# Optimization experiments

Hardware: AMD Instinct MI355X
Metric: run time of the kernel (lower is better)

## Reference

```python
import jax, jax.numpy as jnp
import numpy as np

N = 65536
PT_DIM = 3
ENC_DIM = 512
P = 4096
RADIUS = 0.05
ALPHA = 6.0
SQRT_D = ENC_DIM ** 0.5


def setup_inputs() -> dict:
    key = jax.random.key(0)
    k1, k2, k3 = jax.random.split(key, 3)
    pts = jax.random.normal(k1, (N, PT_DIM), dtype=jnp.float32)
    # Frozen random-feature projection matrices (strict_standard_normal ~ randn)
    A = jax.random.normal(k2, (PT_DIM, ENC_DIM), dtype=jnp.float32) * ALPHA
    B = jax.random.normal(k3, (PT_DIM, P), dtype=jnp.float32) * 1.8
    return {"pts": pts, "A": A, "B": B}


def reference(pts, A, B):
    x = pts / RADIUS                      # (N, 3)
    pA = x @ A                            # (N, d)
    pB = x @ B                            # (N, p)
    cA, sA = jnp.cos(pA), jnp.sin(pA)     # (N, d) each
    eA = jnp.concatenate([cA, sA], axis=-1)          # (N, 2d)
    eB = jnp.concatenate([jnp.cos(pB), jnp.sin(pB)], axis=-1)  # (N, 2p)
    # G = eB @ (eB^T @ eA): contract over N first (small 2p x 2d matrix)
    M = eB.T @ eA                         # (2p, 2d)
    G = eB @ M                            # (N, 2d)
    Gc, Gs = G[:, :ENC_DIM], G[:, ENC_DIM:]
    # complex divide (Gc + i Gs) / (cA + i sA); |cA + i sA|^2 == 1
    den = cA * cA + sA * sA
    re = (Gc * cA + Gs * sA) / den
    im = (Gs * cA - Gc * sA) / den
    # L2-normalize the complex vector per point, scale by sqrt(d)
    nrm = jnp.sqrt(jnp.sum(re * re + im * im, axis=-1, keepdims=True))
    scale = SQRT_D / nrm
    # return real/imag concatenated: (N, 2d)
    return jnp.concatenate([re * scale, im * scale], axis=-1)
```

## Files before the change

kernel.cpp:

```cpp
#include <hip/hip_runtime.h>
#include <hip/hip_bf16.h>
#include <math.h>

typedef __attribute__((ext_vector_type(8))) short bf16x8;
typedef __attribute__((ext_vector_type(4))) float f32x4;

constexpr int NPTS = 65536;
constexpr int ENC  = 512;
constexpr int P    = 4096;
constexpr int JD   = 1024;
constexpr int ID   = 8192;
constexpr int CH   = 8192;
constexpr int NCH  = NPTS / CH;
constexpr int LDK  = 8192;

constexpr float INV_R   = 20.0f;
constexpr float INV2PI  = 0.15915494309189535f;
constexpr float SQRT_D  = 22.627416997969522f;

__device__ __forceinline__ unsigned short f2bf(float f) {
    unsigned int u = __float_as_uint(f);
    u = (u + 0x7FFFu + ((u >> 16) & 1u)) >> 16;
    return (unsigned short)u;
}

__device__ __forceinline__ void sincos_rev(float p, float* s, float* c) {
    float r = p * INV2PI;
    r = r - floorf(r);
    *s = __builtin_amdgcn_sinf(r);
    *c = __builtin_amdgcn_cosf(r);
}

__device__ __forceinline__ void gload16(const void* g, void* l) {
    __builtin_amdgcn_global_load_lds(
        (const __attribute__((address_space(1))) unsigned int*)g,
        (__attribute__((address_space(3))) unsigned int*)l, 16, 0, 0);
}

__global__ __launch_bounds__(256)
void gen_t(const float* __restrict__ pts, const float* __restrict__ A,
           const float* __restrict__ B, unsigned short* __restrict__ eAT,
           unsigned short* __restrict__ eBT, int n0) {
    int idx = blockIdx.x * 256 + threadIdx.x;
    int nh  = idx & (CH / 2 - 1);
    int r   = idx >> 12;
    int nl  = nh * 2;
    int n   = n0 + nl;
    float x0a = pts[n * 3 + 0], x1a = pts[n * 3 + 1], x2a = pts[n * 3 + 2];
    float x0b = pts[n * 3 + 3], x1b = pts[n * 3 + 4], x2b = pts[n * 3 + 5];
    float w0, w1, w2;
    unsigned short *dc, *dsn;
    if (r < ENC) {
        w0 = A[r]; w1 = A[ENC + r]; w2 = A[2 * ENC + r];
        dc  = eAT + (size_t)r * CH + nl;
        dsn = eAT + (size_t)(r + ENC) * CH + nl;
    } else {
        int i = r - ENC;
        w0 = B[i]; w1 = B[P + i]; w2 = B[2 * P + i];
        dc  = eBT + (size_t)i * CH + nl;
        dsn = eBT + (size_t)(i + P) * CH + nl;
    }
    float pa = (x0a * w0 + x1a * w1 + x2a * w2) * INV_R;
    float pb = (x0b * w0 + x1b * w1 + x2b * w2) * INV_R;
    float sa, ca, sb, cb;
    sincos_rev(pa, &sa, &ca);
    sincos_rev(pb, &sb, &cb);
    ushort2 vc; vc.x = f2bf(ca); vc.y = f2bf(cb);
    ushort2 vs; vs.x = f2bf(sa); vs.y = f2bf(sb);
    *(ushort2*)dc  = vc;
    *(ushort2*)dsn = vs;
}

__global__ __launch_bounds__(256)
void gen_b(const float* __restrict__ pts, const float* __restrict__ B,
           unsigned short* __restrict__ eB, int n0) {
    int idx = blockIdx.x * 256 + threadIdx.x;
    int ih = idx & 2047;
    int ln = idx >> 11;
    int i  = ih * 2;
    int n  = n0 + ln;
    float x0 = pts[n * 3 + 0], x1 = pts[n * 3 + 1], x2 = pts[n * 3 + 2];
    float p0 = (x0 * B[i]     + x1 * B[P + i]     + x2 * B[2 * P + i])     * INV_R;
    float p1 = (x0 * B[i + 1] + x1 * B[P + i + 1] + x2 * B[2 * P + i + 1]) * INV_R;
    float s0, c0, s1, c1;
    sincos_rev(p0, &s0, &c0);
    sincos_rev(p1, &s1, &c1);
    ushort2 vc; vc.x = f2bf(c0); vc.y = f2bf(c1);
    ushort2 vs; vs.x = f2bf(s0); vs.y = f2bf(s1);
    *(ushort2*)(eB + (size_t)ln * ID + i)     = vc;
    *(ushort2*)(eB + (size_t)ln * ID + P + i) = vs;
}

template <int BM, int BN, int K, bool ACCUM>
__global__ __launch_bounds__(512, 2)
void gemm_nt(const unsigned short* __restrict__ Ag,
             const unsigned short* __restrict__ Bg,
             float* __restrict__ C, int ldc, int beta) {
    constexpr int BSZ = (BM + BN) * 64;
    constexpr int NA  = BM / 64;
    constexpr int NB  = BN / 64;
    constexpr int NT  = K / 64;
    static_assert(NA + NB == 6, "6 issues/K-tile assumed by vmcnt(6)");
    __shared__ __align__(16) unsigned short lds[3 * BSZ];

    const int tid  = threadIdx.x;
    const int wave = tid >> 6, lane = tid & 63;
    const int mr = lane & 15, q = lane >> 4;
    const int srow = tid >> 3, sslot = tid & 7;
    const int wm = (BM >= BN) ? (wave >> 1) * 64 : (wave & 1) * 64;
    const int wn = (BM >= BN) ? (wave & 1) * 64 : (wave >> 1) * 64;

    const int gx   = gridDim.x;
    const int nwg  = gx * gridDim.y;
    const int flat = blockIdx.y * gx + blockIdx.x;
    const int swz  = (flat & 7) * (nwg >> 3) + (flat >> 3);
    const int m0   = (swz % gx) * BM;
    const int n0   = (swz / gx) * BN;

    const char* aG = (const char*)Ag;
    const char* bG = (const char*)Bg;
    const int ssw = (sslot ^ (srow & 7)) * 16;
    size_t aoff[NA], boff[NB];
#pragma unroll
    for (int j = 0; j < NA; ++j)
        aoff[j] = (size_t)(m0 + j * 64 + srow) * (LDK * 2) + ssw;
#pragma unroll
    for (int j = 0; j < NB; ++j)
        boff[j] = (size_t)(n0 + j * 64 + srow) * (LDK * 2) + ssw;

    unsigned short* bufC  = lds;
    unsigned short* bufN  = lds + BSZ;
    unsigned short* bufN2 = lds + 2 * BSZ;

    auto stage = [&](int idx, unsigned short* buf, size_t kB) {
        if (idx < NA)
            gload16(aG + aoff[idx] + kB, buf + idx * 4096 + wave * 512);
        else
            gload16(bG + boff[idx - NA] + kB,
                    buf + BM * 64 + (idx - NA) * 4096 + wave * 512);
    };

    f32x4 acc[4][4];
#pragma unroll
    for (int a = 0; a < 4; ++a)
#pragma unroll
        for (int b = 0; b < 4; ++b) acc[a][b] = (f32x4){0.f, 0.f, 0.f, 0.f};

#pragma unroll
    for (int i = 0; i < 6; ++i) stage(i, bufC, 0);
#pragma unroll
    for (int i = 0; i < 6; ++i) stage(i, bufN, 128);
    asm volatile("s_waitcnt vmcnt(6)" ::: "memory");
    __builtin_amdgcn_s_barrier();
    __builtin_amdgcn_sched_barrier(0);

    size_t kPre = 256;
#pragma unroll 1
    for (int kt = 0; kt < NT; ++kt) {
        const bool pf = (kt + 2 < NT);
        bf16x8 af[2][4], bfr[2][4];
#pragma unroll
        for (int kk = 0; kk < 2; ++kk) {
#pragma unroll
            for (int mi = 0; mi < 4; ++mi) {
                int m = wm + mi * 16 + mr;
                af[kk][mi] = *(const bf16x8*)(bufC + m * 64 +
                                              (((kk * 4 + q) ^ (m & 7)) * 8));
            }
#pragma unroll
            for (int ni = 0; ni < 4; ++ni) {
                int n = wn + ni * 16 + mr;
                bfr[kk][ni] = *(const bf16x8*)(bufC + BM * 64 + n * 64 +
                                               (((kk * 4 + q) ^ (n & 7)) * 8));
            }
        }
        if (pf) {
#pragma unroll
            for (int i = 0; i < 6; ++i) stage(i, bufN2, kPre);
        }
        __builtin_amdgcn_s_setprio(1);
#pragma unroll
        for (int kk = 0; kk < 2; ++kk)
#pragma unroll
            for (int mi = 0; mi < 4; ++mi)
#pragma unroll
                for (int ni = 0; ni < 4; ++ni)
                    acc[mi][ni] = __builtin_amdgcn_mfma_f32_16x16x32_bf16(
                        af[kk][mi], bfr[kk][ni], acc[mi][ni], 0, 0, 0);
        __builtin_amdgcn_s_setprio(0);
        if (pf)                    asm volatile("s_waitcnt vmcnt(6)" ::: "memory");
        else if (kt + 1 < NT)      asm volatile("s_waitcnt vmcnt(0)" ::: "memory");
        __builtin_amdgcn_s_barrier();
        __builtin_amdgcn_sched_barrier(0);
        unsigned short* t = bufC; bufC = bufN; bufN = bufN2; bufN2 = t;
        kPre += 128;
    }

#pragma unroll
    for (int mi = 0; mi < 4; ++mi)
#pragma unroll
        for (int ni = 0; ni < 4; ++ni)
#pragma unroll
            for (int r = 0; r < 4; ++r) {
                int m = m0 + wm + mi * 16 + q * 4 + r;
                int n = n0 + wn + ni * 16 + mr;
                size_t off = (size_t)m * ldc + n;
                float v = acc[mi][ni][r];
                if (ACCUM) { if (beta) v += C[off]; }
                C[off] = v;
            }
}

__global__ __launch_bounds__(256)
void cvt(const float* __restrict__ src, unsigned short* __restrict__ dst) {
    int idx = blockIdx.x * 256 + threadIdx.x;
    float4 v = ((const float4*)src)[idx];
    ushort4 o;
    o.x = f2bf(v.x); o.y = f2bf(v.y); o.z = f2bf(v.z); o.w = f2bf(v.w);
    ((ushort4*)dst)[idx] = o;
}

__global__ __launch_bounds__(256)
void epi(float* __restrict__ out, const float* __restrict__ pts,
         const float* __restrict__ A) {
    int n = blockIdx.x;
    int t = threadIdx.x;
    float x0 = pts[n * 3 + 0], x1 = pts[n * 3 + 1], x2 = pts[n * 3 + 2];
    float* row = out + (size_t)n * JD;
    float reA[2], imA[2];
    float ssum = 0.f;
#pragma unroll
    for (int u = 0; u < 2; ++u) {
        int j = t + u * 256;
        float pa = (x0 * A[j] + x1 * A[ENC + j] + x2 * A[2 * ENC + j]) * INV_R;
        float s, c;
        sincos_rev(pa, &s, &c);
        float gc = row[j], gs = row[ENC + j];
        float re = gc * c + gs * s;
        float im = gs * c - gc * s;
        reA[u] = re; imA[u] = im;
        ssum += re * re + im * im;
    }
#pragma unroll
    for (int off = 32; off > 0; off >>= 1) ssum += __shfl_down(ssum, off);
    __shared__ float red[4];
    if ((t & 63) == 0) red[t >> 6] = ssum;
    __syncthreads();
    float tot = red[0] + red[1] + red[2] + red[3];
    float scale = SQRT_D / sqrtf(tot);
#pragma unroll
    for (int u = 0; u < 2; ++u) {
        int j = t + u * 256;
        row[j]       = reA[u] * scale;
        row[ENC + j] = imA[u] * scale;
    }
}

extern "C" void kernel_launch(void* const* d_in, const int* in_sizes, int n_in,
                              void* d_out, int out_size, void* d_ws, size_t ws_size,
                              hipStream_t stream) {
    const float* pts = (const float*)d_in[0];
    const float* A   = (const float*)d_in[1];
    const float* B   = (const float*)d_in[2];
    float* out = (float*)d_out;
    char* ws = (char*)d_ws;

    unsigned short* eAT = (unsigned short*)ws;
    unsigned short* eBT = (unsigned short*)(ws + (size_t)JD * CH * 2);
    unsigned short* eBw = (unsigned short*)ws;
    size_t offMT = (size_t)(JD + ID) * CH * 2;
    float* MTf = (float*)(ws + offMT);
    unsigned short* MTb = (unsigned short*)(ws + offMT + (size_t)JD * ID * 4);

    for (int c = 0; c < NCH; ++c) {
        gen_t<<<dim3(73728), 256, 0, stream>>>(pts, A, B, eAT, eBT, c * CH);
        gemm_nt<128, 256, CH, true><<<dim3(8, 32), 512, 0, stream>>>(
            eAT, eBT, MTf, ID, c);
    }
    cvt<<<dim3(8192), 256, 0, stream>>>(MTf, MTb);
    for (int c = 0; c < NCH; ++c) {
        gen_b<<<dim3(65536), 256, 0, stream>>>(pts, B, eBw, c * CH);
        gemm_nt<256, 128, ID, false><<<dim3(32, 8), 512, 0, stream>>>(
            eBw, MTb, out + (size_t)c * CH * JD, JD, 0);
    }
    epi<<<dim3(NPTS), 256, 0, stream>>>(out, pts, A);
}
```

Before: 3.278 ms.

## Use split-K GEMM with atomic accumulation for second-stage product

Replaces the second GEMM (8192x1024 output per chunk, K=8192) with a new kernel that splits K into two halves across blockIdx.z, uses 256x256 tiles with triple-buffered LDS and a grid swizzle, and accumulates partial results with float atomicAdd. Each chunk's output region is now zeroed by a separate kernel before the GEMM. The aim is more blocks in flight (256 instead of 256 smaller tiles with longer K) and better reuse from larger tiles. In exchange it adds atomic traffic and an extra memset pass over the output, and the atomics make the floating-point summation order nondeterministic.

```diff
diff --git a/kernel.cpp b/kernel.cpp
--- a/kernel.cpp
+++ b/kernel.cpp
@@ -211,6 +211,125 @@
             }
 }
 
+__global__ __launch_bounds__(512, 2)
+void gemm_sk(const unsigned short* __restrict__ Ag,
+             const unsigned short* __restrict__ Bg,
+             float* __restrict__ C, int ldc) {
+    constexpr int BK    = 32;
+    constexpr int BSZ   = 512 * BK;
+    constexpr int KHALF = 4096;
+    constexpr int NT    = KHALF / BK;
+    __shared__ __align__(16) unsigned short lds[3 * BSZ];
+
+    const int tid  = threadIdx.x;
+    const int wave = tid >> 6, lane = tid & 63;
+    const int mr = lane & 15, q = lane >> 4;
+    const int wm = (wave >> 1) * 64;
+    const int wn = (wave & 1) * 128;
+
+    const int flat = blockIdx.x + 32 * (blockIdx.y + 4 * blockIdx.z);
+    const int swz  = (flat & 7) * 32 + (flat >> 3);
+    const int m0   = (swz & 31) * 256;
+    const int rest = swz >> 5;
+    const int n0   = (rest & 3) * 256;
+    const int z    = rest >> 2;
+    const size_t kb0 = (size_t)z * KHALF * 2;
+
+    const int L  = tid >> 3;
+    const int S  = tid & 7;
+    const int u  = S ^ (L & 7);
+    const int grow = 2 * L + (u >> 2);
+    const int gk   = (u & 3) * 16;
+    const char* aG = (const char*)Ag;
+    const char* bG = (const char*)Bg;
+    size_t aoff[2], boff[2];
+#pragma unroll
+    for (int j = 0; j < 2; ++j) {
+        aoff[j] = (size_t)(m0 + j * 128 + grow) * (LDK * 2) + kb0 + gk;
+        boff[j] = (size_t)(n0 + j * 128 + grow) * (LDK * 2) + kb0 + gk;
+    }
+
+    unsigned short* bufC  = lds;
+    unsigned short* bufN  = lds + BSZ;
+    unsigned short* bufN2 = lds + 2 * BSZ;
+
+    auto stage = [&](int idx, unsigned short* buf, size_t kB) {
+        if (idx < 2)
+            gload16(aG + aoff[idx] + kB, buf + idx * 4096 + wave * 512);
+        else
+            gload16(bG + boff[idx - 2] + kB,
+                    buf + 8192 + (idx - 2) * 4096 + wave * 512);
+    };
+
+    f32x4 acc[4][8];
+#pragma unroll
+    for (int a = 0; a < 4; ++a)
+#pragma unroll
+        for (int b = 0; b < 8; ++b) acc[a][b] = (f32x4){0.f, 0.f, 0.f, 0.f};
+
+#pragma unroll
+    for (int i = 0; i < 4; ++i) stage(i, bufC, 0);
+#pragma unroll
+    for (int i = 0; i < 4; ++i) stage(i, bufN, 64);
+    asm volatile("s_waitcnt vmcnt(4)" ::: "memory");
+    __builtin_amdgcn_s_barrier();
+    __builtin_amdgcn_sched_barrier(0);
+
+    size_t kPre = 128;
+#pragma unroll 1
+    for (int kt = 0; kt < NT; ++kt) {
+        const bool pf = (kt + 2 < NT);
+        bf16x8 af[4], bfr[8];
+#pragma unroll
+        for (int mi = 0; mi < 4; ++mi) {
+            int m = wm + mi * 16 + mr, Lm = m >> 1;
+            af[mi] = *(const bf16x8*)(bufC + Lm * 64 +
+                                      ((((m & 1) * 4 + q) ^ (Lm & 7)) * 8));
+        }
+#pragma unroll
+        for (int ni = 0; ni < 8; ++ni) {
+            int n = wn + ni * 16 + mr, Ln = n >> 1;
+            bfr[ni] = *(const bf16x8*)(bufC + 8192 + Ln * 64 +
+                                       ((((n & 1) * 4 + q) ^ (Ln & 7)) * 8));
+        }
+        if (pf) {
+#pragma unroll
+            for (int i = 0; i < 4; ++i) stage(i, bufN2, kPre);
+        }
+        __builtin_amdgcn_s_setprio(1);
+#pragma unroll
+        for (int mi = 0; mi < 4; ++mi)
+#pragma unroll
+            for (int ni = 0; ni < 8; ++ni)
+                acc[mi][ni] = __builtin_amdgcn_mfma_f32_16x16x32_bf16(
+                    af[mi], bfr[ni], acc[mi][ni], 0, 0, 0);
+        __builtin_amdgcn_s_setprio(0);
+        if (pf)                    asm volatile("s_waitcnt vmcnt(4)" ::: "memory");
+        else if (kt + 1 < NT)      asm volatile("s_waitcnt vmcnt(0)" ::: "memory");
+        __builtin_amdgcn_s_barrier();
+        __builtin_amdgcn_sched_barrier(0);
+        unsigned short* t = bufC; bufC = bufN; bufN = bufN2; bufN2 = t;
+        kPre += 64;
+    }
+
+#pragma unroll
+    for (int mi = 0; mi < 4; ++mi)
+#pragma unroll
+        for (int ni = 0; ni < 8; ++ni)
+#pragma unroll
+            for (int r = 0; r < 4; ++r) {
+                int m = m0 + wm + mi * 16 + q * 4 + r;
+                int n = n0 + wn + ni * 16 + mr;
+                atomicAdd(&C[(size_t)m * ldc + n], acc[mi][ni][r]);
+            }
+}
+
+__global__ __launch_bounds__(256)
+void zerof(float4* __restrict__ p) {
+    int idx = blockIdx.x * 256 + threadIdx.x;
+    p[idx] = (float4){0.f, 0.f, 0.f, 0.f};
+}
+
 __global__ __launch_bounds__(256)
 void cvt(const float* __restrict__ src, unsigned short* __restrict__ dst) {
     int idx = blockIdx.x * 256 + threadIdx.x;
@@ -280,8 +399,10 @@
     cvt<<<dim3(8192), 256, 0, stream>>>(MTf, MTb);
     for (int c = 0; c < NCH; ++c) {
         gen_b<<<dim3(65536), 256, 0, stream>>>(pts, B, eBw, c * CH);
-        gemm_nt<256, 128, ID, false><<<dim3(32, 8), 512, 0, stream>>>(
-            eBw, MTb, out + (size_t)c * CH * JD, JD, 0);
+        zerof<<<dim3(8192), 256, 0, stream>>>(
+            (float4*)(out + (size_t)c * CH * JD));
+        gemm_sk<<<dim3(32, 4, 2), 512, 0, stream>>>(
+            eBw, MTb, out + (size_t)c * CH * JD, JD);
     }
     epi<<<dim3(NPTS), 256, 0, stream>>>(out, pts, A);
 }
```

After: 3.367 ms. 2.7% more time.

## Quantize first GEMM operands to int8 and use i8 MFMA

Applied to the files above, without the earlier changes.

The sin/cos features feeding the M = eB^T eA reduction over points are now quantized to int8 with scale 127 instead of bf16, and a new int8 MFMA GEMM (16x16x64) accumulates into int32. The int32 result is rescaled by 1/127^2 when it is converted to bf16 for the second GEMM. This halves operand bytes and uses the higher-throughput int8 matrix path for the first GEMM, at the cost of coarser precision (about 7 bits) in the features.

```diff
diff --git a/kernel.cpp b/kernel.cpp
--- a/kernel.cpp
+++ b/kernel.cpp
@@ -4,6 +4,7 @@
 
 typedef __attribute__((ext_vector_type(8))) short bf16x8;
 typedef __attribute__((ext_vector_type(4))) float f32x4;
+typedef __attribute__((ext_vector_type(4))) int   i32x4;
 
 constexpr int NPTS = 65536;
 constexpr int ENC  = 512;
@@ -17,6 +18,7 @@
 constexpr float INV_R   = 20.0f;
 constexpr float INV2PI  = 0.15915494309189535f;
 constexpr float SQRT_D  = 22.627416997969522f;
+constexpr float INV_Q2  = 1.0f / (127.0f * 127.0f);
 
 __device__ __forceinline__ unsigned short f2bf(float f) {
     unsigned int u = __float_as_uint(f);
@@ -39,8 +41,8 @@
 
 __global__ __launch_bounds__(256)
 void gen_t(const float* __restrict__ pts, const float* __restrict__ A,
-           const float* __restrict__ B, unsigned short* __restrict__ eAT,
-           unsigned short* __restrict__ eBT, int n0) {
+           const float* __restrict__ B, signed char* __restrict__ eAT,
+           signed char* __restrict__ eBT, int n0) {
     int idx = blockIdx.x * 256 + threadIdx.x;
     int nh  = idx & (CH / 2 - 1);
     int r   = idx >> 12;
@@ -49,7 +51,7 @@
     float x0a = pts[n * 3 + 0], x1a = pts[n * 3 + 1], x2a = pts[n * 3 + 2];
     float x0b = pts[n * 3 + 3], x1b = pts[n * 3 + 4], x2b = pts[n * 3 + 5];
     float w0, w1, w2;
-    unsigned short *dc, *dsn;
+    signed char *dc, *dsn;
     if (r < ENC) {
         w0 = A[r]; w1 = A[ENC + r]; w2 = A[2 * ENC + r];
         dc  = eAT + (size_t)r * CH + nl;
@@ -65,10 +67,13 @@
     float sa, ca, sb, cb;
     sincos_rev(pa, &sa, &ca);
     sincos_rev(pb, &sb, &cb);
-    ushort2 vc; vc.x = f2bf(ca); vc.y = f2bf(cb);
-    ushort2 vs; vs.x = f2bf(sa); vs.y = f2bf(sb);
-    *(ushort2*)dc  = vc;
-    *(ushort2*)dsn = vs;
+    char2 vc, vs;
+    vc.x = (signed char)__float2int_rn(ca * 127.0f);
+    vc.y = (signed char)__float2int_rn(cb * 127.0f);
+    vs.x = (signed char)__float2int_rn(sa * 127.0f);
+    vs.y = (signed char)__float2int_rn(sb * 127.0f);
+    *(char2*)dc  = vc;
+    *(char2*)dsn = vs;
 }
 
 __global__ __launch_bounds__(256)
@@ -91,6 +96,121 @@
     *(ushort2*)(eB + (size_t)ln * ID + P + i) = vs;
 }
 
+__global__ __launch_bounds__(512, 2)
+void gemm_i8(const signed char* __restrict__ Ag,
+             const signed char* __restrict__ Bg,
+             int* __restrict__ C, int ldc, int beta) {
+    constexpr int BSZB = (128 + 256) * 128;
+    constexpr int NT   = 8192 / 128;
+    __shared__ __align__(16) signed char lds[3 * BSZB];
+
+    const int tid  = threadIdx.x;
+    const int wave = tid >> 6, lane = tid & 63;
+    const int mr = lane & 15, q = lane >> 4;
+    const int srow = tid >> 3, sslot = tid & 7;
+    const int wm = (wave & 1) * 64, wn = (wave >> 1) * 64;
+
+    const int gx   = gridDim.x;
+    const int nwg  = gx * gridDim.y;
+    const int flat = blockIdx.y * gx + blockIdx.x;
+    const int swz  = (flat & 7) * (nwg >> 3) + (flat >> 3);
+    const int m0   = (swz % gx) * 128;
+    const int n0   = (swz / gx) * 256;
+
+    const char* aG = (const char*)Ag;
+    const char* bG = (const char*)Bg;
+    const int ssw = (sslot ^ (srow & 7)) * 16;
+    size_t aoff[2], boff[4];
+#pragma unroll
+    for (int j = 0; j < 2; ++j)
+        aoff[j] = (size_t)(m0 + j * 64 + srow) * LDK + ssw;
+#pragma unroll
+    for (int j = 0; j < 4; ++j)
+        boff[j] = (size_t)(n0 + j * 64 + srow) * LDK + ssw;
+
+    signed char* bufC  = lds;
+    signed char* bufN  = lds + BSZB;
+    signed char* bufN2 = lds + 2 * BSZB;
+
+    auto stage = [&](int idx, signed char* buf, size_t kB) {
+        if (idx < 2)
+            gload16(aG + aoff[idx] + kB, buf + idx * 8192 + tid * 16);
+        else
+            gload16(bG + boff[idx - 2] + kB,
+                    buf + 16384 + (idx - 2) * 8192 + tid * 16);
+    };
+
+    i32x4 acc[4][4];
+#pragma unroll
+    for (int a = 0; a < 4; ++a)
+#pragma unroll
+        for (int b = 0; b < 4; ++b) acc[a][b] = (i32x4){0, 0, 0, 0};
+
+#pragma unroll
+    for (int i = 0; i < 6; ++i) stage(i, bufC, 0);
+#pragma unroll
+    for (int i = 0; i < 6; ++i) stage(i, bufN, 128);
+    asm volatile("s_waitcnt vmcnt(6)" ::: "memory");
+    __builtin_amdgcn_s_barrier();
+    __builtin_amdgcn_sched_barrier(0);
+
+    size_t kPre = 256;
+#pragma unroll 1
+    for (int kt = 0; kt < NT; ++kt) {
+        const bool pf = (kt + 2 < NT);
+        i32x4 af[2][4], bfr[2][4];
+#pragma unroll
+        for (int kk = 0; kk < 2; ++kk) {
+#pragma unroll
+            for (int mi = 0; mi < 4; ++mi) {
+                int m = wm + mi * 16 + mr;
+                af[kk][mi] = *(const i32x4*)(bufC + m * 128 +
+                                             (((kk * 4 + q) ^ (m & 7)) * 16));
+            }
+#pragma unroll
+            for (int ni = 0; ni < 4; ++ni) {
+                int n = wn + ni * 16 + mr;
+                bfr[kk][ni] = *(const i32x4*)(bufC + 16384 + n * 128 +
+                                              (((kk * 4 + q) ^ (n & 7)) * 16));
+            }
+        }
+        if (pf) {
+#pragma unroll
+            for (int i = 0; i < 6; ++i) stage(i, bufN2, kPre);
+        }
+        __builtin_amdgcn_s_setprio(1);
+#pragma unroll
+        for (int kk = 0; kk < 2; ++kk)
+#pragma unroll
+            for (int mi = 0; mi < 4; ++mi)
+#pragma unroll
+                for (int ni = 0; ni < 4; ++ni)
+                    acc[mi][ni] = __builtin_amdgcn_mfma_i32_16x16x64_i8(
+                        af[kk][mi], bfr[kk][ni], acc[mi][ni], 0, 0, 0);
+        __builtin_amdgcn_s_setprio(0);
+        if (pf)                    asm volatile("s_waitcnt vmcnt(6)" ::: "memory");
+        else if (kt + 1 < NT)      asm volatile("s_waitcnt vmcnt(0)" ::: "memory");
+        __builtin_amdgcn_s_barrier();
+        __builtin_amdgcn_sched_barrier(0);
+        signed char* t = bufC; bufC = bufN; bufN = bufN2; bufN2 = t;
+        kPre += 128;
+    }
+
+#pragma unroll
+    for (int mi = 0; mi < 4; ++mi)
+#pragma unroll
+        for (int ni = 0; ni < 4; ++ni)
+#pragma unroll
+            for (int r = 0; r < 4; ++r) {
+                int m = m0 + wm + mi * 16 + q * 4 + r;
+                int n = n0 + wn + ni * 16 + mr;
+                size_t off = (size_t)m * ldc + n;
+                int v = acc[mi][ni][r];
+                if (beta) v += C[off];
+                C[off] = v;
+            }
+}
+
 template <int BM, int BN, int K, bool ACCUM>
 __global__ __launch_bounds__(512, 2)
 void gemm_nt(const unsigned short* __restrict__ Ag,
@@ -212,11 +332,12 @@
 }
 
 __global__ __launch_bounds__(256)
-void cvt(const float* __restrict__ src, unsigned short* __restrict__ dst) {
+void cvt(const int* __restrict__ src, unsigned short* __restrict__ dst) {
     int idx = blockIdx.x * 256 + threadIdx.x;
-    float4 v = ((const float4*)src)[idx];
+    int4 v = ((const int4*)src)[idx];
     ushort4 o;
-    o.x = f2bf(v.x); o.y = f2bf(v.y); o.z = f2bf(v.z); o.w = f2bf(v.w);
+    o.x = f2bf((float)v.x * INV_Q2); o.y = f2bf((float)v.y * INV_Q2);
+    o.z = f2bf((float)v.z * INV_Q2); o.w = f2bf((float)v.w * INV_Q2);
     ((ushort4*)dst)[idx] = o;
 }
 
@@ -265,19 +386,17 @@
     float* out = (float*)d_out;
     char* ws = (char*)d_ws;
 
-    unsigned short* eAT = (unsigned short*)ws;
-    unsigned short* eBT = (unsigned short*)(ws + (size_t)JD * CH * 2);
-    unsigned short* eBw = (unsigned short*)ws;
-    size_t offMT = (size_t)(JD + ID) * CH * 2;
-    float* MTf = (float*)(ws + offMT);
-    unsigned short* MTb = (unsigned short*)(ws + offMT + (size_t)JD * ID * 4);
+    signed char*    eAT8 = (signed char*)ws;
+    signed char*    eBT8 = (signed char*)(ws + ((size_t)8 << 20));
+    unsigned short* eBw  = (unsigned short*)ws;
+    int*            MTi  = (int*)(ws + ((size_t)128 << 20));
+    unsigned short* MTb  = (unsigned short*)(ws + ((size_t)160 << 20));
 
     for (int c = 0; c < NCH; ++c) {
-        gen_t<<<dim3(73728), 256, 0, stream>>>(pts, A, B, eAT, eBT, c * CH);
-        gemm_nt<128, 256, CH, true><<<dim3(8, 32), 512, 0, stream>>>(
-            eAT, eBT, MTf, ID, c);
-    }
-    cvt<<<dim3(8192), 256, 0, stream>>>(MTf, MTb);
+        gen_t<<<dim3(73728), 256, 0, stream>>>(pts, A, B, eAT8, eBT8, c * CH);
+        gemm_i8<<<dim3(8, 32), 512, 0, stream>>>(eAT8, eBT8, MTi, ID, c);
+    }
+    cvt<<<dim3(8192), 256, 0, stream>>>(MTi, MTb);
     for (int c = 0; c < NCH; ++c) {
         gen_b<<<dim3(65536), 256, 0, stream>>>(pts, B, eBw, c * CH);
         gemm_nt<256, 128, ID, false><<<dim3(32, 8), 512, 0, stream>>>(
```

After: 2.858 ms. 12.8% less time.
